# Kernel optimization log

Measured on AMD Instinct MI355X. Metric: run time of the kernel, lower is better.

Reference implementation:

```python
import jax, jax.numpy as jnp
import numpy as np

N = 8192
F_IN = 128
F_OUT = 128


def setup_inputs() -> dict:
    key = jax.random.key(0)
    k1, k2, k3, k4, k5 = jax.random.split(key, 5)
    x = jax.random.normal(k1, (N, F_IN), dtype=jnp.float32)
    adj = jax.random.uniform(k2, (N, N), dtype=jnp.float32)
    kernel = jax.random.normal(k3, (F_IN, F_OUT), dtype=jnp.float32) * 0.05
    bias = jax.random.normal(k4, (F_OUT,), dtype=jnp.float32) * 0.05
    beta = jax.random.uniform(k5, (N,), dtype=jnp.float32)
    return {"x": x, "adj": adj, "kernel": kernel, "bias": bias, "beta": beta}


def reference(x, adj, kernel, bias, beta):
    # torch: diag(1/(adj.sum(1)+beta)) @ (adj + diag(beta)) @ x @ kernel + bias
    # (adj + diag(beta)) @ x  ==  adj @ x + beta[:, None] * x  (no NxN temp)
    inv_deg = 1.0 / (jnp.sum(adj, axis=1) + beta)        # [N]
    agg = adj @ x + beta[:, None] * x                     # [N, F_in]
    out = (inv_deg[:, None] * agg) @ kernel + bias        # [N, F_out]
    return out
```

## Files before the change

kernel.cpp:

```cpp
#include <hip/hip_runtime.h>

#define NN 8192
#define FD 128
#define BK 128

typedef float f32x4 __attribute__((ext_vector_type(4)));
typedef short short8 __attribute__((ext_vector_type(8)));
typedef unsigned short ushort4v __attribute__((ext_vector_type(4)));
typedef unsigned short ushort8v __attribute__((ext_vector_type(8)));

__device__ __forceinline__ unsigned short f2bf(float f) {
  unsigned int u = __builtin_bit_cast(unsigned int, f);
  u += 0x7fffu + ((u >> 16) & 1u);
  return (unsigned short)(u >> 16);
}
__device__ __forceinline__ float bf2f(unsigned short h) {
  unsigned int u = ((unsigned int)h) << 16;
  return __builtin_bit_cast(float, u);
}

__global__ __launch_bounds__(256) void xk_kernel(
    const float* __restrict__ x, const float* __restrict__ kern,
    unsigned short* __restrict__ bfrag, unsigned short* __restrict__ xk_rm) {
  __shared__ __align__(16) unsigned short kl[FD * FD];
  __shared__ __align__(16) float xl[16 * FD];
  const int t = threadIdx.x;
  const int row0 = blockIdx.x * 16;

  #pragma unroll
  for (int j = 0; j < 16; ++j) {
    int idx = (j * 256 + t) * 4;
    f32x4 kv = *(const f32x4*)&kern[idx];
    ushort4v kw;
    #pragma unroll
    for (int q = 0; q < 4; ++q) kw[q] = f2bf(kv[q]);
    *(ushort4v*)&kl[idx] = kw;
  }
  #pragma unroll
  for (int j = 0; j < 2; ++j) {
    int idx = (j * 256 + t) * 4;
    *(f32x4*)&xl[idx] = *(const f32x4*)&x[(size_t)row0 * FD + idx];
  }
  __syncthreads();

  const int r0 = (t >> 5) * 2;
  const int c0 = (t & 31) * 4;
  float acc[2][4] = {};
  #pragma unroll 4
  for (int k = 0; k < FD; ++k) {
    ushort4v kq = *(const ushort4v*)&kl[k * FD + c0];
    float kv[4];
    #pragma unroll
    for (int q = 0; q < 4; ++q) kv[q] = bf2f(kq[q]);
    float x0 = xl[r0 * FD + k];
    float x1 = xl[(r0 + 1) * FD + k];
    #pragma unroll
    for (int q = 0; q < 4; ++q) {
      acc[0][q] += x0 * kv[q];
      acc[1][q] += x1 * kv[q];
    }
  }
  #pragma unroll
  for (int i = 0; i < 2; ++i) {
    const int r = row0 + r0 + i;
    const int kt = r >> 5;
    const int lhi = ((r >> 3) & 3) * 16;
    const int j = r & 7;
    ushort4v ow;
    #pragma unroll
    for (int q = 0; q < 4; ++q) {
      const int c = c0 + q;
      unsigned short bv = f2bf(acc[i][q]);
      ow[q] = bv;
      bfrag[(((size_t)kt * 8 + (c >> 4)) * 64 + (lhi + (c & 15))) * 8 + j] = bv;
    }
    *(ushort4v*)&xk_rm[(size_t)r * FD + c0] = ow;
  }
}

#define PREF(Lr, stp)                                                         \
  do {                                                                        \
    _Pragma("unroll") for (int i = 0; i < 4; ++i)                             \
        Lr[i] = *(const f32x4*)(ap + (size_t)(i * 8) * NN + (stp) * BK);      \
  } while (0)

#define STAGE(Lr, buf)                                                        \
  do {                                                                        \
    _Pragma("unroll") for (int i = 0; i < 4; ++i) {                           \
      ushort4v cw;                                                            \
      _Pragma("unroll") for (int q = 0; q < 4; ++q) cw[q] = f2bf(Lr[i][q]);   \
      rs[i] += Lr[i][0] + Lr[i][1] + Lr[i][2] + Lr[i][3];                     \
      const int row_l = i * 8 + srow;                                         \
      *(ushort4v*)&sA[buf][row_l * 128 +                                      \
                           (scol ^ ((row_l & 7) << 3))] = cw;                 \
    }                                                                         \
  } while (0)

#define LOAD_B(stp)                                                           \
  do {                                                                        \
    const int ktg = kt0 + (stp) * 4;                                          \
    _Pragma("unroll") for (int kk = 0; kk < 4; ++kk)                          \
        _Pragma("unroll") for (int ci = 0; ci < 2; ++ci)                      \
            Bf[kk * 2 + ci] = *(const ushort8v*)(bp +                         \
                (((size_t)(ktg + kk) * 8 + (w * 2 + ci)) << 9));              \
  } while (0)

#define MFMA_STEP(buf)                                                        \
  do {                                                                        \
    __builtin_amdgcn_s_setprio(1);                                            \
    _Pragma("unroll") for (int kk = 0; kk < 4; ++kk) {                        \
      short8 aF[2];                                                           \
      _Pragma("unroll") for (int mf = 0; mf < 2; ++mf) {                      \
        const int r = mf * 16 + (l & 15);                                     \
        const int colu = kk * 32 + (l >> 4) * 8;                              \
        aF[mf] = *(const short8*)&sA[buf][r * 128 +                           \
                                          (colu ^ ((r & 7) << 3))];           \
      }                                                                       \
      _Pragma("unroll") for (int mf = 0; mf < 2; ++mf)                        \
          _Pragma("unroll") for (int ci = 0; ci < 2; ++ci)                    \
              acc[mf][ci] = __builtin_amdgcn_mfma_f32_16x16x32_bf16(          \
                  aF[mf], Bf[kk * 2 + ci], acc[mf][ci], 0, 0, 0);             \
    }                                                                         \
    __builtin_amdgcn_s_setprio(0);                                            \
  } while (0)

#define LDS_BARRIER()                                                         \
  do {                                                                        \
    asm volatile("s_waitcnt lgkmcnt(0)" ::: "memory");                        \
    __builtin_amdgcn_sched_barrier(0);                                        \
    __builtin_amdgcn_s_barrier();                                             \
  } while (0)

template <int S>
__global__ __launch_bounds__(256, 4) void gcn_mm(
    const float* __restrict__ adj, const unsigned short* __restrict__ bfrag,
    unsigned short* __restrict__ parts, float* __restrict__ rowpart) {
  constexpr int KW = NN / S;
  constexpr int NS = KW / BK;
  __shared__ unsigned short sA[2][32 * 128];

  const int t = threadIdx.x;
  const int l = t & 63;
  const int w = t >> 6;
  const int b = blockIdx.x;
  const int s = b & (S - 1);
  const int row0 = (b / S) * 32;
  const int kbase = s * KW;
  const int kt0 = s * (KW / 32);

  const int srow = t >> 5;
  const int scol = (t & 31) * 4;
  const float* ap = adj + (size_t)(row0 + srow) * NN + kbase + scol;
  const unsigned short* bp = bfrag + (size_t)l * 8;

  f32x4 LrA[4], LrB[4];
  ushort8v Bf[8];
  f32x4 acc[2][2] = {};
  float rs[4] = {};

  PREF(LrA, 0);
  STAGE(LrA, 0);
  PREF(LrB, 1);
  LDS_BARRIER();

  for (int st = 0; st < NS; st += 2) {
    LOAD_B(st);
    if (st + 2 < NS) PREF(LrA, st + 2);
    __builtin_amdgcn_sched_barrier(0);
    MFMA_STEP(0);
    STAGE(LrB, 1);
    LDS_BARRIER();
    LOAD_B(st + 1);
    if (st + 3 < NS) PREF(LrB, st + 3);
    __builtin_amdgcn_sched_barrier(0);
    MFMA_STEP(1);
    if (st + 2 < NS) STAGE(LrA, 0);
    LDS_BARRIER();
  }

  #pragma unroll
  for (int i = 0; i < 4; ++i) {
    rs[i] += __shfl_xor(rs[i], 1);
    rs[i] += __shfl_xor(rs[i], 2);
    rs[i] += __shfl_xor(rs[i], 4);
    rs[i] += __shfl_xor(rs[i], 8);
    rs[i] += __shfl_xor(rs[i], 16);
  }
  if ((l & 31) == 0) {
    #pragma unroll
    for (int i = 0; i < 4; ++i)
      rowpart[(size_t)s * NN + row0 + i * 8 + srow] = rs[i];
  }

  unsigned short* pp = parts + ((size_t)s * NN + row0) * FD + w * 32;
  #pragma unroll
  for (int mf = 0; mf < 2; ++mf)
    #pragma unroll
    for (int ci = 0; ci < 2; ++ci)
      #pragma unroll
      for (int j = 0; j < 4; ++j) {
        const int r = mf * 16 + ((l >> 4) << 2) + j;
        pp[(size_t)r * FD + ci * 16 + (l & 15)] = f2bf(acc[mf][ci][j]);
      }
}

__global__ __launch_bounds__(256) void gcn_fin(
    const unsigned short* __restrict__ parts, const float* __restrict__ rowpart,
    const unsigned short* __restrict__ xk_rm, const float* __restrict__ beta,
    const float* __restrict__ bias, float* __restrict__ out, int S) {
  const int t = threadIdx.x;
  const int r = blockIdx.x * 16 + (t >> 4);
  const int c0 = (t & 15) * 8;

  float rsum = 0.f;
  for (int s = 0; s < S; ++s) rsum += rowpart[(size_t)s * NN + r];
  const float bt = beta[r];
  const float inv = 1.0f / (rsum + bt);

  float a[8] = {0.f, 0.f, 0.f, 0.f, 0.f, 0.f, 0.f, 0.f};
  for (int s = 0; s < S; ++s) {
    ushort8v pv = *(const ushort8v*)&parts[((size_t)s * NN + r) * FD + c0];
    #pragma unroll
    for (int q = 0; q < 8; ++q) a[q] += bf2f(pv[q]);
  }
  ushort8v xv = *(const ushort8v*)&xk_rm[(size_t)r * FD + c0];
  f32x4 o0, o1;
  #pragma unroll
  for (int q = 0; q < 4; ++q) {
    o0[q] = (a[q] + bt * bf2f(xv[q])) * inv + bias[c0 + q];
    o1[q] = (a[4 + q] + bt * bf2f(xv[4 + q])) * inv + bias[c0 + 4 + q];
  }
  *(f32x4*)&out[(size_t)r * FD + c0] = o0;
  *(f32x4*)&out[(size_t)r * FD + c0 + 4] = o1;
}

extern "C" void kernel_launch(void* const* d_in, const int* in_sizes, int n_in,
                              void* d_out, int out_size, void* d_ws, size_t ws_size,
                              hipStream_t stream) {
  const float* x    = (const float*)d_in[0];
  const float* adj  = (const float*)d_in[1];
  const float* kern = (const float*)d_in[2];
  const float* bias = (const float*)d_in[3];
  const float* beta = (const float*)d_in[4];
  float* out = (float*)d_out;

  char* ws = (char*)d_ws;
  unsigned short* bfrag = (unsigned short*)ws;
  unsigned short* xk_rm = (unsigned short*)(ws + (size_t)NN * FD * 2);
  const size_t off_rowpart = (size_t)NN * FD * 4;
  float* rowpart = (float*)(ws + off_rowpart);
  const size_t off_parts = off_rowpart + (size_t)8 * NN * 4;
  unsigned short* parts = (unsigned short*)(ws + off_parts);

  int S = 8;
  while (S > 1 && off_parts + (size_t)S * NN * FD * 2 > ws_size) S >>= 1;

  hipLaunchKernelGGL(xk_kernel, dim3(NN / 16), dim3(256), 0, stream,
                     x, kern, bfrag, xk_rm);

  dim3 blk(256);
  switch (S) {
    case 8: hipLaunchKernelGGL(gcn_mm<8>, dim3(256 * 8), blk, 0, stream, adj, bfrag, parts, rowpart); break;
    case 4: hipLaunchKernelGGL(gcn_mm<4>, dim3(256 * 4), blk, 0, stream, adj, bfrag, parts, rowpart); break;
    case 2: hipLaunchKernelGGL(gcn_mm<2>, dim3(256 * 2), blk, 0, stream, adj, bfrag, parts, rowpart); break;
    default: hipLaunchKernelGGL(gcn_mm<1>, dim3(256), blk, 0, stream, adj, bfrag, parts, rowpart); break;
  }

  hipLaunchKernelGGL(gcn_fin, dim3(NN / 16), dim3(256), 0, stream,
                     parts, rowpart, xk_rm, beta, bias, out, S);
}
```

Before: 80.73 us.

## Stream adjacency tiles into a 4-deep LDS ring via direct global-to-LDS loads

Replaces the register-staged prefetch, bf16 conversion and LDS store of the fp32 adjacency tile with global_load_lds DMA into a 4-slot fp32 ring in shared memory. The bf16 conversion moves to the consume side using v_cvt_pk_bf16_f32, and the row sums are computed from the LDS fragments and reduced through a small shared array. B fragments are double-buffered in registers and barriers wait on vmcnt instead of lgkmcnt. The aim is to free VGPRs and VALU work from staging and to keep more loads in flight. In exchange it doubles LDS traffic because tiles are stored as fp32, and it lowers the occupancy hint from 4 to 2 blocks per CU.

```diff
diff --git a/kernel.cpp b/kernel.cpp
--- a/kernel.cpp
+++ b/kernel.cpp
@@ -3,11 +3,13 @@
 #define NN 8192
 #define FD 128
 #define BK 128
+#define NRING 4
 
 typedef float f32x4 __attribute__((ext_vector_type(4)));
 typedef short short8 __attribute__((ext_vector_type(8)));
 typedef unsigned short ushort4v __attribute__((ext_vector_type(4)));
 typedef unsigned short ushort8v __attribute__((ext_vector_type(8)));
+typedef unsigned int uint4v __attribute__((ext_vector_type(4)));
 
 __device__ __forceinline__ unsigned short f2bf(float f) {
   unsigned int u = __builtin_bit_cast(unsigned int, f);
@@ -78,66 +80,72 @@
   }
 }
 
-#define PREF(Lr, stp)                                                         \
-  do {                                                                        \
-    _Pragma("unroll") for (int i = 0; i < 4; ++i)                             \
-        Lr[i] = *(const f32x4*)(ap + (size_t)(i * 8) * NN + (stp) * BK);      \
-  } while (0)
-
-#define STAGE(Lr, buf)                                                        \
-  do {                                                                        \
-    _Pragma("unroll") for (int i = 0; i < 4; ++i) {                           \
-      ushort4v cw;                                                            \
-      _Pragma("unroll") for (int q = 0; q < 4; ++q) cw[q] = f2bf(Lr[i][q]);   \
-      rs[i] += Lr[i][0] + Lr[i][1] + Lr[i][2] + Lr[i][3];                     \
-      const int row_l = i * 8 + srow;                                         \
-      *(ushort4v*)&sA[buf][row_l * 128 +                                      \
-                           (scol ^ ((row_l & 7) << 3))] = cw;                 \
+#define DMA_A(stp, buf)                                                       \
+  do {                                                                        \
+    _Pragma("unroll") for (int c = 0; c < 4; ++c) {                           \
+      const float* g = ag[c] + (size_t)(stp) * BK;                            \
+      __builtin_amdgcn_global_load_lds(                                       \
+          (const __attribute__((address_space(1))) void*)g,                   \
+          (__attribute__((address_space(3))) void*)                           \
+              &ring[buf][(w * 4 + c) * 256],                                  \
+          16, 0, 0);                                                          \
     }                                                                         \
   } while (0)
 
-#define LOAD_B(stp)                                                           \
+#define LOAD_B(stp, Bf)                                                       \
   do {                                                                        \
     const int ktg = kt0 + (stp) * 4;                                          \
     _Pragma("unroll") for (int kk = 0; kk < 4; ++kk)                          \
-        _Pragma("unroll") for (int ci = 0; ci < 2; ++ci)                      \
-            Bf[kk * 2 + ci] = *(const ushort8v*)(bp +                         \
-                (((size_t)(ktg + kk) * 8 + (w * 2 + ci)) << 9));              \
-  } while (0)
-
-#define MFMA_STEP(buf)                                                        \
-  do {                                                                        \
-    __builtin_amdgcn_s_setprio(1);                                            \
+      _Pragma("unroll") for (int ci = 0; ci < 2; ++ci)                        \
+        Bf[kk * 2 + ci] = *(const ushort8v*)(bp +                             \
+            (((size_t)(ktg + kk) * 8 + (w * 2 + ci)) << 9));                  \
+  } while (0)
+
+#define WAITBAR()                                                             \
+  do {                                                                        \
+    asm volatile("s_waitcnt vmcnt(12)" ::: "memory");                         \
+    __builtin_amdgcn_sched_barrier(0);                                        \
+    __builtin_amdgcn_s_barrier();                                             \
+    __builtin_amdgcn_sched_barrier(0);                                        \
+  } while (0)
+
+#define CONSUME(buf, Bf)                                                      \
+  do {                                                                        \
+    const float* sb = &ring[buf][0];                                          \
     _Pragma("unroll") for (int kk = 0; kk < 4; ++kk) {                        \
       short8 aF[2];                                                           \
       _Pragma("unroll") for (int mf = 0; mf < 2; ++mf) {                      \
-        const int r = mf * 16 + (l & 15);                                     \
-        const int colu = kk * 32 + (l >> 4) * 8;                              \
-        aF[mf] = *(const short8*)&sA[buf][r * 128 +                           \
-                                          (colu ^ ((r & 7) << 3))];           \
+        const int row = (l & 15) + 16 * mf;                                   \
+        const int u0 = (l >> 4) * 2 + kk * 8;                                 \
+        f32x4 lo = *(const f32x4*)&sb[row * BK + ((u0 ^ (row & 7)) * 4)];     \
+        f32x4 hi = *(const f32x4*)&sb[row * BK + (((u0 + 1) ^ (row & 7)) * 4)];\
+        unsigned int w0, w1, w2, w3;                                          \
+        asm("v_cvt_pk_bf16_f32 %0, %1, %2" : "=v"(w0) : "v"(lo[0]), "v"(lo[1]));\
+        asm("v_cvt_pk_bf16_f32 %0, %1, %2" : "=v"(w1) : "v"(lo[2]), "v"(lo[3]));\
+        asm("v_cvt_pk_bf16_f32 %0, %1, %2" : "=v"(w2) : "v"(hi[0]), "v"(hi[1]));\
+        asm("v_cvt_pk_bf16_f32 %0, %1, %2" : "=v"(w3) : "v"(hi[2]), "v"(hi[3]));\
+        uint4v uw = {w0, w1, w2, w3};                                         \
+        aF[mf] = __builtin_bit_cast(short8, uw);                              \
+        if (kk == w)                                                          \
+          rs[mf] += lo[0] + lo[1] + lo[2] + lo[3] +                           \
+                    hi[0] + hi[1] + hi[2] + hi[3];                            \
       }                                                                       \
       _Pragma("unroll") for (int mf = 0; mf < 2; ++mf)                        \
-          _Pragma("unroll") for (int ci = 0; ci < 2; ++ci)                    \
-              acc[mf][ci] = __builtin_amdgcn_mfma_f32_16x16x32_bf16(          \
-                  aF[mf], Bf[kk * 2 + ci], acc[mf][ci], 0, 0, 0);             \
+        _Pragma("unroll") for (int ci = 0; ci < 2; ++ci)                      \
+          acc[mf][ci] = __builtin_amdgcn_mfma_f32_16x16x32_bf16(              \
+              aF[mf], Bf[kk * 2 + ci], acc[mf][ci], 0, 0, 0);                 \
     }                                                                         \
-    __builtin_amdgcn_s_setprio(0);                                            \
-  } while (0)
-
-#define LDS_BARRIER()                                                         \
-  do {                                                                        \
-    asm volatile("s_waitcnt lgkmcnt(0)" ::: "memory");                        \
-    __builtin_amdgcn_sched_barrier(0);                                        \
-    __builtin_amdgcn_s_barrier();                                             \
   } while (0)
 
 template <int S>
-__global__ __launch_bounds__(256, 4) void gcn_mm(
+__global__ __launch_bounds__(256, 2) void gcn_mm(
     const float* __restrict__ adj, const unsigned short* __restrict__ bfrag,
     unsigned short* __restrict__ parts, float* __restrict__ rowpart) {
   constexpr int KW = NN / S;
   constexpr int NS = KW / BK;
-  __shared__ unsigned short sA[2][32 * 128];
+  static_assert(NS >= 4 && (NS % 2) == 0, "ring needs NS>=4 even");
+  __shared__ float ring[NRING][32 * BK];
+  __shared__ float rsx[4][2][16];
 
   const int t = threadIdx.x;
   const int l = t & 63;
@@ -148,48 +156,51 @@
   const int kbase = s * KW;
   const int kt0 = s * (KW / 32);
 
-  const int srow = t >> 5;
-  const int scol = (t & 31) * 4;
-  const float* ap = adj + (size_t)(row0 + srow) * NN + kbase + scol;
+  const float* ag[4];
+  #pragma unroll
+  for (int c = 0; c < 4; ++c) {
+    const int row = 8 * w + 2 * c + (l >> 5);
+    const int u = (l & 31) ^ (row & 7);
+    ag[c] = adj + (size_t)(row0 + row) * NN + kbase + u * 4;
+  }
   const unsigned short* bp = bfrag + (size_t)l * 8;
 
-  f32x4 LrA[4], LrB[4];
-  ushort8v Bf[8];
+  ushort8v BfA[8], BfB[8];
   f32x4 acc[2][2] = {};
-  float rs[4] = {};
-
-  PREF(LrA, 0);
-  STAGE(LrA, 0);
-  PREF(LrB, 1);
-  LDS_BARRIER();
-
-  for (int st = 0; st < NS; st += 2) {
-    LOAD_B(st);
-    if (st + 2 < NS) PREF(LrA, st + 2);
+  float rs[2] = {0.f, 0.f};
+
+  DMA_A(0, 0);
+  DMA_A(1, 1);
+  DMA_A(2, 2);
+  LOAD_B(0, BfA);
+
+  for (int j = 0; j < NS; j += 2) {
+    LOAD_B((j + 1 < NS ? j + 1 : NS - 1), BfB);
+    WAITBAR();
+    if (j + 3 < NS) DMA_A(j + 3, (j + 3) & 3);
     __builtin_amdgcn_sched_barrier(0);
-    MFMA_STEP(0);
-    STAGE(LrB, 1);
-    LDS_BARRIER();
-    LOAD_B(st + 1);
-    if (st + 3 < NS) PREF(LrB, st + 3);
+    CONSUME(j & 3, BfA);
+    LOAD_B((j + 2 < NS ? j + 2 : NS - 1), BfA);
+    WAITBAR();
+    if (j + 4 < NS) DMA_A(j + 4, (j + 4) & 3);
     __builtin_amdgcn_sched_barrier(0);
-    MFMA_STEP(1);
-    if (st + 2 < NS) STAGE(LrA, 0);
-    LDS_BARRIER();
-  }
-
-  #pragma unroll
-  for (int i = 0; i < 4; ++i) {
-    rs[i] += __shfl_xor(rs[i], 1);
-    rs[i] += __shfl_xor(rs[i], 2);
-    rs[i] += __shfl_xor(rs[i], 4);
-    rs[i] += __shfl_xor(rs[i], 8);
-    rs[i] += __shfl_xor(rs[i], 16);
-  }
-  if ((l & 31) == 0) {
-    #pragma unroll
-    for (int i = 0; i < 4; ++i)
-      rowpart[(size_t)s * NN + row0 + i * 8 + srow] = rs[i];
+    CONSUME((j + 1) & 3, BfB);
+  }
+
+  #pragma unroll
+  for (int mf = 0; mf < 2; ++mf) {
+    rs[mf] += __shfl_xor(rs[mf], 16);
+    rs[mf] += __shfl_xor(rs[mf], 32);
+  }
+  if (l < 16) {
+    rsx[w][0][l] = rs[0];
+    rsx[w][1][l] = rs[1];
+  }
+  __syncthreads();
+  if (t < 32) {
+    float tot = rsx[0][t >> 4][t & 15] + rsx[1][t >> 4][t & 15] +
+                rsx[2][t >> 4][t & 15] + rsx[3][t >> 4][t & 15];
+    rowpart[(size_t)s * NN + row0 + t] = tot;
   }
 
   unsigned short* pp = parts + ((size_t)s * NN + row0) * FD + w * 32;
@@ -198,9 +209,9 @@
     #pragma unroll
     for (int ci = 0; ci < 2; ++ci)
       #pragma unroll
-      for (int j = 0; j < 4; ++j) {
-        const int r = mf * 16 + ((l >> 4) << 2) + j;
-        pp[(size_t)r * FD + ci * 16 + (l & 15)] = f2bf(acc[mf][ci][j]);
+      for (int jj = 0; jj < 4; ++jj) {
+        const int r = mf * 16 + ((l >> 4) << 2) + jj;
+        pp[(size_t)r * FD + ci * 16 + (l & 15)] = f2bf(acc[mf][ci][jj]);
       }
 }
 
```

New measurement: 87.44 us. 8.3% more time.

## Replace split-K matmul and finalize kernels with fused full-K row-block kernel

Applied to the files above, without the earlier changes.

Drops the split-K decomposition: each 512-thread block now covers 16 full rows of adj across the whole K range with 8 waves, each owning 16 output columns. Row sums, normalization, the beta term and bias are applied in the epilogue, so the bf16 partials buffer and the separate finalize launch go away. In exchange there are only 512 blocks, each running a long serial K loop. B fragments are reused less per adj tile, and the loop may expose more load latency.

```diff
diff --git a/kernel.cpp b/kernel.cpp
--- a/kernel.cpp
+++ b/kernel.cpp
@@ -2,7 +2,9 @@
 
 #define NN 8192
 #define FD 128
-#define BK 128
+#define BKF 256
+#define NS (NN / BKF)
+#define RPB 16
 
 typedef float f32x4 __attribute__((ext_vector_type(4)));
 typedef short short8 __attribute__((ext_vector_type(8)));
@@ -80,46 +82,35 @@
 
 #define PREF(Lr, stp)                                                         \
   do {                                                                        \
-    _Pragma("unroll") for (int i = 0; i < 4; ++i)                             \
-        Lr[i] = *(const f32x4*)(ap + (size_t)(i * 8) * NN + (stp) * BK);      \
+    Lr[0] = *(const f32x4*)(ap + (size_t)(stp) * BKF);                        \
+    Lr[1] = *(const f32x4*)(ap + (size_t)(stp) * BKF + 128);                  \
   } while (0)
 
 #define STAGE(Lr, buf)                                                        \
   do {                                                                        \
-    _Pragma("unroll") for (int i = 0; i < 4; ++i) {                           \
+    _Pragma("unroll") for (int i = 0; i < 2; ++i) {                           \
       ushort4v cw;                                                            \
       _Pragma("unroll") for (int q = 0; q < 4; ++q) cw[q] = f2bf(Lr[i][q]);   \
-      rs[i] += Lr[i][0] + Lr[i][1] + Lr[i][2] + Lr[i][3];                     \
-      const int row_l = i * 8 + srow;                                         \
-      *(ushort4v*)&sA[buf][row_l * 128 +                                      \
-                           (scol ^ ((row_l & 7) << 3))] = cw;                 \
+      rs += Lr[i][0] + Lr[i][1] + Lr[i][2] + Lr[i][3];                        \
+      const int cc = scol + i * 128;                                          \
+      *(ushort4v*)&sA[buf][srow * 256 + (cc ^ sxor)] = cw;                    \
     }                                                                         \
   } while (0)
 
 #define LOAD_B(stp)                                                           \
   do {                                                                        \
-    const int ktg = kt0 + (stp) * 4;                                          \
-    _Pragma("unroll") for (int kk = 0; kk < 4; ++kk)                          \
-        _Pragma("unroll") for (int ci = 0; ci < 2; ++ci)                      \
-            Bf[kk * 2 + ci] = *(const ushort8v*)(bp +                         \
-                (((size_t)(ktg + kk) * 8 + (w * 2 + ci)) << 9));              \
+    const int ktg = (stp) * 8;                                                \
+    _Pragma("unroll") for (int h = 0; h < 8; ++h)                             \
+      Bf[h] = *(const ushort8v*)(bp + (((size_t)(ktg + h) * 8 + w) << 9));    \
   } while (0)
 
 #define MFMA_STEP(buf)                                                        \
   do {                                                                        \
     __builtin_amdgcn_s_setprio(1);                                            \
-    _Pragma("unroll") for (int kk = 0; kk < 4; ++kk) {                        \
-      short8 aF[2];                                                           \
-      _Pragma("unroll") for (int mf = 0; mf < 2; ++mf) {                      \
-        const int r = mf * 16 + (l & 15);                                     \
-        const int colu = kk * 32 + (l >> 4) * 8;                              \
-        aF[mf] = *(const short8*)&sA[buf][r * 128 +                           \
-                                          (colu ^ ((r & 7) << 3))];           \
-      }                                                                       \
-      _Pragma("unroll") for (int mf = 0; mf < 2; ++mf)                        \
-          _Pragma("unroll") for (int ci = 0; ci < 2; ++ci)                    \
-              acc[mf][ci] = __builtin_amdgcn_mfma_f32_16x16x32_bf16(          \
-                  aF[mf], Bf[kk * 2 + ci], acc[mf][ci], 0, 0, 0);             \
+    _Pragma("unroll") for (int h = 0; h < 8; ++h) {                           \
+      const int colu = (h * 32 + (l >> 4) * 8) ^ axor;                        \
+      short8 aF = *(const short8*)&sA[buf][arow * 256 + colu];                \
+      acc = __builtin_amdgcn_mfma_f32_16x16x32_bf16(aF, Bf[h], acc, 0, 0, 0); \
     }                                                                         \
     __builtin_amdgcn_s_setprio(0);                                            \
   } while (0)
@@ -129,34 +120,36 @@
     asm volatile("s_waitcnt lgkmcnt(0)" ::: "memory");                        \
     __builtin_amdgcn_sched_barrier(0);                                        \
     __builtin_amdgcn_s_barrier();                                             \
-  } while (0)
-
-template <int S>
-__global__ __launch_bounds__(256, 4) void gcn_mm(
+    __builtin_amdgcn_sched_barrier(0);                                        \
+  } while (0)
+
+__global__ __launch_bounds__(512, 4) void gcn_fused(
     const float* __restrict__ adj, const unsigned short* __restrict__ bfrag,
-    unsigned short* __restrict__ parts, float* __restrict__ rowpart) {
-  constexpr int KW = NN / S;
-  constexpr int NS = KW / BK;
-  __shared__ unsigned short sA[2][32 * 128];
+    const unsigned short* __restrict__ xk_rm, const float* __restrict__ beta,
+    const float* __restrict__ bias, float* __restrict__ out) {
+  __shared__ unsigned short sA[2][RPB * 256];
+  __shared__ float rs_lds[RPB];
+  __shared__ float inv_lds[RPB];
+  __shared__ float beta_lds[RPB];
 
   const int t = threadIdx.x;
   const int l = t & 63;
   const int w = t >> 6;
-  const int b = blockIdx.x;
-  const int s = b & (S - 1);
-  const int row0 = (b / S) * 32;
-  const int kbase = s * KW;
-  const int kt0 = s * (KW / 32);
+  const int row0 = blockIdx.x * RPB;
 
   const int srow = t >> 5;
   const int scol = (t & 31) * 4;
-  const float* ap = adj + (size_t)(row0 + srow) * NN + kbase + scol;
+  const int sxor = (srow & 7) << 3;
+  const float* ap = adj + (size_t)(row0 + srow) * NN + scol;
+
+  const int arow = l & 15;
+  const int axor = (arow & 7) << 3;
   const unsigned short* bp = bfrag + (size_t)l * 8;
 
-  f32x4 LrA[4], LrB[4];
+  f32x4 LrA[2], LrB[2];
   ushort8v Bf[8];
-  f32x4 acc[2][2] = {};
-  float rs[4] = {};
+  f32x4 acc = {0.f, 0.f, 0.f, 0.f};
+  float rs = 0.f;
 
   PREF(LrA, 0);
   STAGE(LrA, 0);
@@ -178,60 +171,29 @@
     LDS_BARRIER();
   }
 
-  #pragma unroll
-  for (int i = 0; i < 4; ++i) {
-    rs[i] += __shfl_xor(rs[i], 1);
-    rs[i] += __shfl_xor(rs[i], 2);
-    rs[i] += __shfl_xor(rs[i], 4);
-    rs[i] += __shfl_xor(rs[i], 8);
-    rs[i] += __shfl_xor(rs[i], 16);
-  }
-  if ((l & 31) == 0) {
-    #pragma unroll
-    for (int i = 0; i < 4; ++i)
-      rowpart[(size_t)s * NN + row0 + i * 8 + srow] = rs[i];
-  }
-
-  unsigned short* pp = parts + ((size_t)s * NN + row0) * FD + w * 32;
-  #pragma unroll
-  for (int mf = 0; mf < 2; ++mf)
-    #pragma unroll
-    for (int ci = 0; ci < 2; ++ci)
-      #pragma unroll
-      for (int j = 0; j < 4; ++j) {
-        const int r = mf * 16 + ((l >> 4) << 2) + j;
-        pp[(size_t)r * FD + ci * 16 + (l & 15)] = f2bf(acc[mf][ci][j]);
-      }
-}
-
-__global__ __launch_bounds__(256) void gcn_fin(
-    const unsigned short* __restrict__ parts, const float* __restrict__ rowpart,
-    const unsigned short* __restrict__ xk_rm, const float* __restrict__ beta,
-    const float* __restrict__ bias, float* __restrict__ out, int S) {
-  const int t = threadIdx.x;
-  const int r = blockIdx.x * 16 + (t >> 4);
-  const int c0 = (t & 15) * 8;
-
-  float rsum = 0.f;
-  for (int s = 0; s < S; ++s) rsum += rowpart[(size_t)s * NN + r];
-  const float bt = beta[r];
-  const float inv = 1.0f / (rsum + bt);
-
-  float a[8] = {0.f, 0.f, 0.f, 0.f, 0.f, 0.f, 0.f, 0.f};
-  for (int s = 0; s < S; ++s) {
-    ushort8v pv = *(const ushort8v*)&parts[((size_t)s * NN + r) * FD + c0];
-    #pragma unroll
-    for (int q = 0; q < 8; ++q) a[q] += bf2f(pv[q]);
-  }
-  ushort8v xv = *(const ushort8v*)&xk_rm[(size_t)r * FD + c0];
-  f32x4 o0, o1;
-  #pragma unroll
-  for (int q = 0; q < 4; ++q) {
-    o0[q] = (a[q] + bt * bf2f(xv[q])) * inv + bias[c0 + q];
-    o1[q] = (a[4 + q] + bt * bf2f(xv[4 + q])) * inv + bias[c0 + 4 + q];
-  }
-  *(f32x4*)&out[(size_t)r * FD + c0] = o0;
-  *(f32x4*)&out[(size_t)r * FD + c0 + 4] = o1;
+  rs += __shfl_xor(rs, 1, 32);
+  rs += __shfl_xor(rs, 2, 32);
+  rs += __shfl_xor(rs, 4, 32);
+  rs += __shfl_xor(rs, 8, 32);
+  rs += __shfl_xor(rs, 16, 32);
+  if ((l & 31) == 0) rs_lds[srow] = rs;
+  __syncthreads();
+  if (t < RPB) {
+    const float bt = beta[row0 + t];
+    beta_lds[t] = bt;
+    inv_lds[t] = 1.0f / (rs_lds[t] + bt);
+  }
+  __syncthreads();
+
+  const int cg = w * 16 + (l & 15);
+  const float bias_v = bias[cg];
+  #pragma unroll
+  for (int j = 0; j < 4; ++j) {
+    const int r = ((l >> 4) << 2) + j;
+    const float xkv = bf2f(xk_rm[(size_t)(row0 + r) * FD + cg]);
+    out[(size_t)(row0 + r) * FD + cg] =
+        (acc[j] + beta_lds[r] * xkv) * inv_lds[r] + bias_v;
+  }
 }
 
 extern "C" void kernel_launch(void* const* d_in, const int* in_sizes, int n_in,
@@ -247,25 +209,9 @@
   char* ws = (char*)d_ws;
   unsigned short* bfrag = (unsigned short*)ws;
   unsigned short* xk_rm = (unsigned short*)(ws + (size_t)NN * FD * 2);
-  const size_t off_rowpart = (size_t)NN * FD * 4;
-  float* rowpart = (float*)(ws + off_rowpart);
-  const size_t off_parts = off_rowpart + (size_t)8 * NN * 4;
-  unsigned short* parts = (unsigned short*)(ws + off_parts);
-
-  int S = 8;
-  while (S > 1 && off_parts + (size_t)S * NN * FD * 2 > ws_size) S >>= 1;
 
   hipLaunchKernelGGL(xk_kernel, dim3(NN / 16), dim3(256), 0, stream,
                      x, kern, bfrag, xk_rm);
-
-  dim3 blk(256);
-  switch (S) {
-    case 8: hipLaunchKernelGGL(gcn_mm<8>, dim3(256 * 8), blk, 0, stream, adj, bfrag, parts, rowpart); break;
-    case 4: hipLaunchKernelGGL(gcn_mm<4>, dim3(256 * 4), blk, 0, stream, adj, bfrag, parts, rowpart); break;
-    case 2: hipLaunchKernelGGL(gcn_mm<2>, dim3(256 * 2), blk, 0, stream, adj, bfrag, parts, rowpart); break;
-    default: hipLaunchKernelGGL(gcn_mm<1>, dim3(256), blk, 0, stream, adj, bfrag, parts, rowpart); break;
-  }
-
-  hipLaunchKernelGGL(gcn_fin, dim3(NN / 16), dim3(256), 0, stream,
-                     parts, rowpart, xk_rm, beta, bias, out, S);
-}
+  hipLaunchKernelGGL(gcn_fused, dim3(NN / RPB), dim3(512), 0, stream,
+                     adj, bfrag, xk_rm, beta, bias, out);
+}
```

After: 95.57 us. 18.4% more time.
